# Kernel optimization log

Hardware: AMD Instinct MI355X
Metric: run time of the kernel (lower is better)

## Reference

```python
import jax, jax.numpy as jnp
import numpy as np

LN_EPS = 1e-5  # torch nn.LayerNorm default


def setup_inputs() -> dict:
    key = jax.random.key(0)
    kx, kw = jax.random.split(key)
    tokens, d_in, d_out = 8192, 4096, 16384
    x = jax.random.normal(kx, (tokens, d_in), dtype=jnp.float32)
    # nn.Linear weight layout: [out_features, in_features]
    W = jax.random.normal(kw, (d_out, d_in), dtype=jnp.float32) * (1.0 / np.sqrt(d_in))
    return {"x": x, "W": W}


def reference(x, W):
    # LayerNorm over last dim, no affine params (elementwise_affine=False)
    mean = jnp.mean(x, axis=-1, keepdims=True)
    var = jnp.mean(jnp.square(x - mean), axis=-1, keepdims=True)  # biased, as torch LN
    xn = (x - mean) * jax.lax.rsqrt(var + LN_EPS)
    # Linear (no bias): [tokens, d_in] @ [d_in, d_out]
    y = jnp.einsum("td,od->to", xn, W)
    return jax.nn.sigmoid(y)
```

## Files before the change

### kernel.cpp

```cpp
#include <hip/hip_runtime.h>
#include <hip/hip_bf16.h>
#include <stdint.h>

#define TOKENS 8192
#define DIN    4096
#define DOUT   16384

#define BM 256
#define BN 256
#define BKT 64
#define NT (DIN / BKT)
#define NJ (NT / 2)

typedef short s16x8 __attribute__((ext_vector_type(8)));
typedef float f32x4 __attribute__((ext_vector_type(4)));

#define AS1 __attribute__((address_space(1)))
#define AS3 __attribute__((address_space(3)))
#define VMCNT(n)  asm volatile("s_waitcnt vmcnt(" #n ")" ::: "memory")
#define BAR()     __builtin_amdgcn_s_barrier()

__device__ __forceinline__ unsigned short f2bf(float f) {
  unsigned int u = __float_as_uint(f);
  u += 0x7fffu + ((u >> 16) & 1u);
  return (unsigned short)(u >> 16);
}

__global__ __launch_bounds__(256) void ln_kernel(const float* __restrict__ x,
                                                 unsigned short* __restrict__ xn) {
  const int row = blockIdx.x;
  const float4* xr = reinterpret_cast<const float4*>(x + (size_t)row * DIN);
  float4 v[4];
  float sum = 0.f, ssq = 0.f;
#pragma unroll
  for (int i = 0; i < 4; ++i) {
    v[i] = xr[threadIdx.x + i * 256];
    sum += v[i].x + v[i].y + v[i].z + v[i].w;
    ssq += v[i].x * v[i].x + v[i].y * v[i].y + v[i].z * v[i].z + v[i].w * v[i].w;
  }
#pragma unroll
  for (int off = 32; off > 0; off >>= 1) {
    sum += __shfl_xor(sum, off, 64);
    ssq += __shfl_xor(ssq, off, 64);
  }
  __shared__ float red[8];
  const int wid = threadIdx.x >> 6;
  if ((threadIdx.x & 63) == 0) { red[wid] = sum; red[wid + 4] = ssq; }
  __syncthreads();
  sum = red[0] + red[1] + red[2] + red[3];
  ssq = red[4] + red[5] + red[6] + red[7];
  const float mean = sum * (1.f / DIN);
  const float var  = ssq * (1.f / DIN) - mean * mean;
  const float rs   = rsqrtf(var + 1e-5f);
  ushort4* xo = reinterpret_cast<ushort4*>(xn + (size_t)row * DIN);
#pragma unroll
  for (int i = 0; i < 4; ++i) {
    ushort4 o;
    o.x = f2bf((v[i].x - mean) * rs);
    o.y = f2bf((v[i].y - mean) * rs);
    o.z = f2bf((v[i].z - mean) * rs);
    o.w = f2bf((v[i].w - mean) * rs);
    xo[threadIdx.x + i * 256] = o;
  }
}

__global__ __launch_bounds__(256) void cvt_kernel(const float* __restrict__ W,
                                                  unsigned short* __restrict__ Wb) {
  const size_t i = (size_t)blockIdx.x * 256 + threadIdx.x;
  float4 v = reinterpret_cast<const float4*>(W)[i];
  ushort4 o;
  o.x = f2bf(v.x); o.y = f2bf(v.y); o.z = f2bf(v.z); o.w = f2bf(v.w);
  reinterpret_cast<ushort4*>(Wb)[i] = o;
}

__global__ __launch_bounds__(512, 2) void gemm_sig(const unsigned short* __restrict__ A,
                                                   const unsigned short* __restrict__ B,
                                                   float* __restrict__ C) {
  __shared__ unsigned short Asl[2 * 256 * 64];
  __shared__ unsigned short Bsl[2 * 256 * 64];

  const int bid = blockIdx.x;
  const int cpx = gridDim.x >> 3;
  const int swz = (bid & 7) * cpx + (bid >> 3);
  const int bm = swz & 31;
  const int bn = swz >> 5;

  const int tid  = threadIdx.x;
  const int wid  = tid >> 6;
  const int lane = tid & 63;
  const int wr = wid >> 2, wc = wid & 3;

  const unsigned short* gA = A + (size_t)bm * BM * DIN;
  const unsigned short* gB = B + (size_t)bn * BN * DIN;

  const int l8 = lane >> 3, l7 = lane & 7;
  const int csw = l7 ^ l8;
  const unsigned short* sA = gA + (size_t)(wid * 8 + l8) * DIN + csw * 8;
  const unsigned short* sB = gB + (size_t)(wid * 8 + l8) * DIN + csw * 8;
  const int dOfs = wid * 512;

#define STG_Aq(p, q, kt) __builtin_amdgcn_global_load_lds( \
    (const AS1 void*)(sA + (size_t)(q) * 64 * DIN + (size_t)(kt) * BKT), \
    (AS3 void*)(Asl + ((p) * 256 + (q) * 64) * 64 + dOfs), 16, 0, 0)
#define STG_Bq(p, q, kt) __builtin_amdgcn_global_load_lds( \
    (const AS1 void*)(sB + (size_t)(q) * 64 * DIN + (size_t)(kt) * BKT), \
    (AS3 void*)(Bsl + ((p) * 256 + (q) * 64) * 64 + dOfs), 16, 0, 0)

  int aO[8], bO[4], slt[2];
#pragma unroll
  for (int m = 0; m < 8; ++m) aO[m] = (wr * 128 + m * 16 + (lane & 15)) * 64;
#pragma unroll
  for (int n = 0; n < 4; ++n) bO[n] = (wc * 64 + n * 16 + (lane & 15)) * 64;
  slt[0] = ((lane >> 4) ^ l7) * 8;
  slt[1] = (((lane >> 4) + 4) ^ l7) * 8;

  s16x8 af[4], bf0[4], bf1[4];
  f32x4 acc[8][4] = {};

#define RD_A(p, mb4, kh) do { _Pragma("unroll") for (int mm = 0; mm < 4; ++mm) \
    af[mm] = *reinterpret_cast<const s16x8*>(Asl + (p) * 16384 + aO[(mb4) + mm] + slt[kh]); } while (0)
#define RD_B(p, kh, dst) do { _Pragma("unroll") for (int nn = 0; nn < 4; ++nn) \
    dst[nn] = *reinterpret_cast<const s16x8*>(Bsl + (p) * 16384 + bO[nn] + slt[kh]); } while (0)
#define MM(mb4, bfr) do { _Pragma("unroll") for (int mm = 0; mm < 4; ++mm) \
    _Pragma("unroll") for (int nn = 0; nn < 4; ++nn) \
      acc[(mb4) + mm][nn] = __builtin_amdgcn_mfma_f32_16x16x32_bf16(af[mm], bfr[nn], acc[(mb4) + mm][nn], 0, 0, 0); } while (0)
#define PRIO1() __builtin_amdgcn_s_setprio(1)
#define PRIO0() __builtin_amdgcn_s_setprio(0)

  STG_Aq(0, 0, 0); STG_Aq(0, 1, 0); STG_Aq(0, 2, 0); STG_Aq(0, 3, 0);
  STG_Bq(0, 0, 0); STG_Bq(0, 1, 0); STG_Bq(0, 2, 0); STG_Bq(0, 3, 0);
  STG_Aq(1, 0, 1); STG_Aq(1, 2, 1);
  STG_Bq(1, 0, 1); STG_Bq(1, 1, 1); STG_Bq(1, 2, 1); STG_Bq(1, 3, 1);
  VMCNT(6); BAR();

  for (int j = 0; j < NJ - 1; ++j) {
    const int t1 = 2 * j + 1, t2 = 2 * j + 2, t3 = 2 * j + 3;
    VMCNT(8); RD_A(0, 0, 0); RD_B(0, 0, bf0);
    STG_Aq(1, 1, t1); STG_Aq(1, 3, t1);
    BAR(); PRIO1(); MM(0, bf0); PRIO0(); BAR();
    VMCNT(8); RD_A(0, 0, 1); RD_B(0, 1, bf1);
    BAR(); PRIO1(); MM(0, bf1); PRIO0(); BAR();
    VMCNT(8); RD_A(0, 4, 0);
    STG_Bq(0, 0, t2); STG_Bq(0, 1, t2); STG_Bq(0, 2, t2); STG_Bq(0, 3, t2);
    STG_Aq(0, 0, t2); STG_Aq(0, 2, t2);
    BAR(); PRIO1(); MM(4, bf0); PRIO0(); BAR();
    VMCNT(8); RD_A(0, 4, 1);
    BAR(); PRIO1(); MM(4, bf1); PRIO0(); BAR();
    VMCNT(8); RD_A(1, 0, 0); RD_B(1, 0, bf0);
    STG_Aq(0, 1, t2); STG_Aq(0, 3, t2);
    BAR(); PRIO1(); MM(0, bf0); PRIO0(); BAR();
    VMCNT(8); RD_A(1, 0, 1); RD_B(1, 1, bf1);
    BAR(); PRIO1(); MM(0, bf1); PRIO0(); BAR();
    VMCNT(8); RD_A(1, 4, 0);
    STG_Bq(1, 0, t3); STG_Bq(1, 1, t3); STG_Bq(1, 2, t3); STG_Bq(1, 3, t3);
    STG_Aq(1, 0, t3); STG_Aq(1, 2, t3);
    BAR(); PRIO1(); MM(4, bf0); PRIO0(); BAR();
    VMCNT(8); RD_A(1, 4, 1);
    BAR(); PRIO1(); MM(4, bf1); PRIO0(); BAR();
  }

  {
    const int t1 = NT - 1;
    VMCNT(8); RD_A(0, 0, 0); RD_B(0, 0, bf0);
    STG_Aq(1, 1, t1); STG_Aq(1, 3, t1);
    BAR(); PRIO1(); MM(0, bf0); PRIO0(); BAR();
    VMCNT(8); RD_A(0, 0, 1); RD_B(0, 1, bf1);
    BAR(); PRIO1(); MM(0, bf1); PRIO0(); BAR();
    VMCNT(8); RD_A(0, 4, 0);
    BAR(); PRIO1(); MM(4, bf0); PRIO0(); BAR();
    VMCNT(2); RD_A(0, 4, 1);
    BAR(); PRIO1(); MM(4, bf1); PRIO0(); BAR();
    VMCNT(2); RD_A(1, 0, 0); RD_B(1, 0, bf0);
    BAR(); PRIO1(); MM(0, bf0); PRIO0(); BAR();
    VMCNT(0); RD_A(1, 0, 1); RD_B(1, 1, bf1);
    BAR(); PRIO1(); MM(0, bf1); PRIO0(); BAR();
    VMCNT(0); RD_A(1, 4, 0);
    BAR(); PRIO1(); MM(4, bf0); PRIO0(); BAR();
    VMCNT(0); RD_A(1, 4, 1);
    BAR(); PRIO1(); MM(4, bf1); PRIO0();
  }

#undef STG_Aq
#undef STG_Bq
#undef RD_A
#undef RD_B
#undef MM

  const int crow0 = bm * BM + wr * 128 + (lane >> 4) * 4;
  const int ccol0 = bn * BN + wc * 64 + (lane & 15);
#pragma unroll
  for (int m = 0; m < 8; ++m)
#pragma unroll
    for (int n = 0; n < 4; ++n)
#pragma unroll
      for (int jj = 0; jj < 4; ++jj) {
        const float v = acc[m][n][jj];
        C[(size_t)(crow0 + m * 16 + jj) * DOUT + (ccol0 + n * 16)] = 1.f / (1.f + __expf(-v));
      }
}

extern "C" void kernel_launch(void* const* d_in, const int* in_sizes, int n_in,
                              void* d_out, int out_size, void* d_ws, size_t ws_size,
                              hipStream_t stream) {
  const float* x = (const float*)d_in[0];
  const float* W = (const float*)d_in[1];
  float* out = (float*)d_out;

  unsigned short* xn = (unsigned short*)d_ws;
  unsigned short* Wb = xn + (size_t)TOKENS * DIN;

  ln_kernel<<<TOKENS, 256, 0, stream>>>(x, xn);
  cvt_kernel<<<((size_t)DOUT * DIN) / 1024, 256, 0, stream>>>(W, Wb);
  gemm_sig<<<(TOKENS / BM) * (DOUT / BN), 512, 0, stream>>>(xn, Wb, out);
}
```

Baseline: 1.337 ms.

## Double-buffer A fragments to overlap LDS reads with MFMA phases

```diff
diff --git a/kernel.cpp b/kernel.cpp
--- a/kernel.cpp
+++ b/kernel.cpp
@@ -114,16 +114,16 @@
   slt[0] = ((lane >> 4) ^ l7) * 8;
   slt[1] = (((lane >> 4) + 4) ^ l7) * 8;
 
-  s16x8 af[4], bf0[4], bf1[4];
+  s16x8 afX[4], afY[4], bf0[4], bf1[4];
   f32x4 acc[8][4] = {};
 
-#define RD_A(p, mb4, kh) do { _Pragma("unroll") for (int mm = 0; mm < 4; ++mm) \
-    af[mm] = *reinterpret_cast<const s16x8*>(Asl + (p) * 16384 + aO[(mb4) + mm] + slt[kh]); } while (0)
+#define RD_A(p, mb4, kh, dst) do { _Pragma("unroll") for (int mm = 0; mm < 4; ++mm) \
+    dst[mm] = *reinterpret_cast<const s16x8*>(Asl + (p) * 16384 + aO[(mb4) + mm] + slt[kh]); } while (0)
 #define RD_B(p, kh, dst) do { _Pragma("unroll") for (int nn = 0; nn < 4; ++nn) \
     dst[nn] = *reinterpret_cast<const s16x8*>(Bsl + (p) * 16384 + bO[nn] + slt[kh]); } while (0)
-#define MM(mb4, bfr) do { _Pragma("unroll") for (int mm = 0; mm < 4; ++mm) \
+#define MM(mb4, afr, bfr) do { _Pragma("unroll") for (int mm = 0; mm < 4; ++mm) \
     _Pragma("unroll") for (int nn = 0; nn < 4; ++nn) \
-      acc[(mb4) + mm][nn] = __builtin_amdgcn_mfma_f32_16x16x32_bf16(af[mm], bfr[nn], acc[(mb4) + mm][nn], 0, 0, 0); } while (0)
+      acc[(mb4) + mm][nn] = __builtin_amdgcn_mfma_f32_16x16x32_bf16(afr[mm], bfr[nn], acc[(mb4) + mm][nn], 0, 0, 0); } while (0)
 #define PRIO1() __builtin_amdgcn_s_setprio(1)
 #define PRIO0() __builtin_amdgcn_s_setprio(0)
 
@@ -132,52 +132,52 @@
   STG_Aq(1, 0, 1); STG_Aq(1, 2, 1);
   STG_Bq(1, 0, 1); STG_Bq(1, 1, 1); STG_Bq(1, 2, 1); STG_Bq(1, 3, 1);
   VMCNT(6); BAR();
+  RD_A(0, 0, 0, afX); RD_B(0, 0, bf0);
 
   for (int j = 0; j < NJ - 1; ++j) {
     const int t1 = 2 * j + 1, t2 = 2 * j + 2, t3 = 2 * j + 3;
-    VMCNT(8); RD_A(0, 0, 0); RD_B(0, 0, bf0);
+    VMCNT(8); RD_A(0, 0, 1, afY); RD_B(0, 1, bf1);
     STG_Aq(1, 1, t1); STG_Aq(1, 3, t1);
-    BAR(); PRIO1(); MM(0, bf0); PRIO0(); BAR();
-    VMCNT(8); RD_A(0, 0, 1); RD_B(0, 1, bf1);
-    BAR(); PRIO1(); MM(0, bf1); PRIO0(); BAR();
-    VMCNT(8); RD_A(0, 4, 0);
+    BAR(); PRIO1(); MM(0, afX, bf0); PRIO0(); BAR();
+    VMCNT(8); RD_A(0, 4, 0, afX);
+    BAR(); PRIO1(); MM(0, afY, bf1); PRIO0(); BAR();
+    VMCNT(8); RD_A(0, 4, 1, afY);
     STG_Bq(0, 0, t2); STG_Bq(0, 1, t2); STG_Bq(0, 2, t2); STG_Bq(0, 3, t2);
     STG_Aq(0, 0, t2); STG_Aq(0, 2, t2);
-    BAR(); PRIO1(); MM(4, bf0); PRIO0(); BAR();
-    VMCNT(8); RD_A(0, 4, 1);
-    BAR(); PRIO1(); MM(4, bf1); PRIO0(); BAR();
-    VMCNT(8); RD_A(1, 0, 0); RD_B(1, 0, bf0);
+    BAR(); PRIO1(); MM(4, afX, bf0); PRIO0(); BAR();
+    VMCNT(8); RD_A(1, 0, 0, afX); RD_B(1, 0, bf0);
+    BAR(); PRIO1(); MM(4, afY, bf1); PRIO0(); BAR();
+    VMCNT(8); RD_A(1, 0, 1, afY); RD_B(1, 1, bf1);
     STG_Aq(0, 1, t2); STG_Aq(0, 3, t2);
-    BAR(); PRIO1(); MM(0, bf0); PRIO0(); BAR();
-    VMCNT(8); RD_A(1, 0, 1); RD_B(1, 1, bf1);
-    BAR(); PRIO1(); MM(0, bf1); PRIO0(); BAR();
-    VMCNT(8); RD_A(1, 4, 0);
+    BAR(); PRIO1(); MM(0, afX, bf0); PRIO0(); BAR();
+    VMCNT(8); RD_A(1, 4, 0, afX);
+    BAR(); PRIO1(); MM(0, afY, bf1); PRIO0(); BAR();
+    VMCNT(8); RD_A(1, 4, 1, afY);
     STG_Bq(1, 0, t3); STG_Bq(1, 1, t3); STG_Bq(1, 2, t3); STG_Bq(1, 3, t3);
     STG_Aq(1, 0, t3); STG_Aq(1, 2, t3);
-    BAR(); PRIO1(); MM(4, bf0); PRIO0(); BAR();
-    VMCNT(8); RD_A(1, 4, 1);
-    BAR(); PRIO1(); MM(4, bf1); PRIO0(); BAR();
+    BAR(); PRIO1(); MM(4, afX, bf0); PRIO0(); BAR();
+    VMCNT(8); RD_A(0, 0, 0, afX); RD_B(0, 0, bf0);
+    BAR(); PRIO1(); MM(4, afY, bf1); PRIO0(); BAR();
   }
 
   {
     const int t1 = NT - 1;
-    VMCNT(8); RD_A(0, 0, 0); RD_B(0, 0, bf0);
+    VMCNT(8); RD_A(0, 0, 1, afY); RD_B(0, 1, bf1);
     STG_Aq(1, 1, t1); STG_Aq(1, 3, t1);
-    BAR(); PRIO1(); MM(0, bf0); PRIO0(); BAR();
-    VMCNT(8); RD_A(0, 0, 1); RD_B(0, 1, bf1);
-    BAR(); PRIO1(); MM(0, bf1); PRIO0(); BAR();
-    VMCNT(8); RD_A(0, 4, 0);
-    BAR(); PRIO1(); MM(4, bf0); PRIO0(); BAR();
-    VMCNT(2); RD_A(0, 4, 1);
-    BAR(); PRIO1(); MM(4, bf1); PRIO0(); BAR();
-    VMCNT(2); RD_A(1, 0, 0); RD_B(1, 0, bf0);
-    BAR(); PRIO1(); MM(0, bf0); PRIO0(); BAR();
-    VMCNT(0); RD_A(1, 0, 1); RD_B(1, 1, bf1);
-    BAR(); PRIO1(); MM(0, bf1); PRIO0(); BAR();
-    VMCNT(0); RD_A(1, 4, 0);
-    BAR(); PRIO1(); MM(4, bf0); PRIO0(); BAR();
-    VMCNT(0); RD_A(1, 4, 1);
-    BAR(); PRIO1(); MM(4, bf1); PRIO0();
+    BAR(); PRIO1(); MM(0, afX, bf0); PRIO0(); BAR();
+    VMCNT(8); RD_A(0, 4, 0, afX);
+    BAR(); PRIO1(); MM(0, afY, bf1); PRIO0(); BAR();
+    VMCNT(8); RD_A(0, 4, 1, afY);
+    BAR(); PRIO1(); MM(4, afX, bf0); PRIO0(); BAR();
+    VMCNT(2); RD_A(1, 0, 0, afX); RD_B(1, 0, bf0);
+    BAR(); PRIO1(); MM(4, afY, bf1); PRIO0(); BAR();
+    VMCNT(2); RD_A(1, 0, 1, afY); RD_B(1, 1, bf1);
+    BAR(); PRIO1(); MM(0, afX, bf0); PRIO0(); BAR();
+    VMCNT(0); RD_A(1, 4, 0, afX);
+    BAR(); PRIO1(); MM(0, afY, bf1); PRIO0(); BAR();
+    VMCNT(0); RD_A(1, 4, 1, afY);
+    BAR(); PRIO1(); MM(4, afX, bf0); PRIO0(); BAR();
+    PRIO1(); MM(4, afY, bf1); PRIO0();
   }
 
 #undef STG_Aq
```

After: 1.283 ms. 1.04x faster.
